# Optimization experiments

Measured on AMD Instinct MI355X. Metric: run time of the kernel, lower is better.

Reference implementation:

```python
import jax, jax.numpy as jnp
import numpy as np

DIM, DEPTH, DH, CH, SH = 512, 2, 64, 2, 8
B, T, N = 8, 1024, 2048
CI, SI, FF = CH * DH, SH * DH, 4 * DIM


def layer_norm(x, w, b, eps=1e-5):
    m = jnp.mean(x, -1, keepdims=True)
    v = jnp.var(x, -1, keepdims=True)
    return (x - m) * jax.lax.rsqrt(v + eps) * w + b


def rotate_half(x):
    # interleaved pairs: (x0,x1) -> (-x1,x0)
    x1, x2 = x[..., 0::2], x[..., 1::2]
    return jnp.stack((-x2, x1), axis=-1).reshape(x.shape)


def apply_rot(freqs, x):
    return x * jnp.cos(freqs) + rotate_half(x) * jnp.sin(freqs)


def split_heads(x, h):
    b, t, _ = x.shape
    return x.reshape(b, t, h, -1).transpose(0, 2, 1, 3)


def merge_heads(x):
    b, h, t, d = x.shape
    return x.transpose(0, 2, 1, 3).reshape(b, t, h * d)


def rotary_attn(q, k, v, q_pos, k_pos, heads, mask=None):
    # q:(B,Tq,H*Dh), k/v:(B,Tk,H*Dh), pos:(B,T,Dh); rotate_value=False -> v untouched
    qh, kh, vh = split_heads(q, heads), split_heads(k, heads), split_heads(v, heads)
    qh = apply_rot(q_pos[:, None], qh)
    kh = apply_rot(k_pos[:, None], kh)
    scores = jnp.einsum('bhqd,bhkd->bhqk', qh, kh) * (DH ** -0.5)
    if mask is not None:
        scores = jnp.where(mask, scores, jnp.finfo(scores.dtype).min)
    attn = jax.nn.softmax(scores, axis=-1)
    return merge_heads(jnp.einsum('bhqk,bhkd->bhqd', attn, vh))


def _forward(bin_queries, bin_time_emb, encoder_latents, latent_time_emb,
             ca_lnq_w, ca_lnq_b, ca_lnc_w, ca_lnc_b, ca_wq, ca_wkv, ca_wo, ca_bo,
             sa_ln_w, sa_ln_b, sa_wqkv, sa_wo, sa_bo,
             ffn_ln_w, ffn_ln_b, ffn_w1, ffn_b1, ffn_w2, ffn_b2):
    Tq = bin_queries.shape[1]
    mask = jnp.tril(jnp.ones((Tq, Tq), dtype=bool))[None, None]  # (1,1,T,T) causal
    x = bin_queries
    for l in range(DEPTH):
        # 1) rotary cross-attention to history latents
        xn = layer_norm(x, ca_lnq_w[l], ca_lnq_b[l])
        cn = layer_norm(encoder_latents, ca_lnc_w[l], ca_lnc_b[l])
        q = xn @ ca_wq[l]
        k, v = jnp.split(cn @ ca_wkv[l], 2, axis=-1)
        x = x + rotary_attn(q, k, v, bin_time_emb, latent_time_emb, CH) @ ca_wo[l] + ca_bo[l]
        # 2) causal rotary self-attention over bin queries
        xn = layer_norm(x, sa_ln_w[l], sa_ln_b[l])
        q, k, v = jnp.split(xn @ sa_wqkv[l], 3, axis=-1)
        x = x + rotary_attn(q, k, v, bin_time_emb, bin_time_emb, SH, mask) @ sa_wo[l] + sa_bo[l]
        # 3) pre-LN FFN with GEGLU (mult=4), dropout off in eval
        h = layer_norm(x, ffn_ln_w[l], ffn_ln_b[l])
        a, g = jnp.split(h @ ffn_w1[l] + ffn_b1[l], 2, axis=-1)
        x = x + (a * jax.nn.gelu(g, approximate=False)) @ ffn_w2[l] + ffn_b2[l]
    return x


def setup_inputs() -> dict:
    key = jax.random.key(0)
    ks = jax.random.split(key, 12)
    n = lambda i, shape, s: jax.random.normal(ks[i], shape, dtype=jnp.float32) * s
    return {
        'bin_queries': n(0, (B, T, DIM), 1.0),
        'bin_time_emb': n(1, (B, T, DH), 1.0),
        'encoder_latents': n(2, (B, N, DIM), 1.0),
        'latent_time_emb': n(3, (B, N, DH), 1.0),
        'ca_lnq_w': jnp.ones((DEPTH, DIM)), 'ca_lnq_b': jnp.zeros((DEPTH, DIM)),
        'ca_lnc_w': jnp.ones((DEPTH, DIM)), 'ca_lnc_b': jnp.zeros((DEPTH, DIM)),
        'ca_wq': n(4, (DEPTH, DIM, CI), 0.02), 'ca_wkv': n(5, (DEPTH, DIM, 2 * CI), 0.02),
        'ca_wo': n(6, (DEPTH, CI, DIM), 0.02), 'ca_bo': jnp.zeros((DEPTH, DIM)),
        'sa_ln_w': jnp.ones((DEPTH, DIM)), 'sa_ln_b': jnp.zeros((DEPTH, DIM)),
        'sa_wqkv': n(7, (DEPTH, DIM, 3 * SI), 0.02), 'sa_wo': n(8, (DEPTH, SI, DIM), 0.02),
        'sa_bo': jnp.zeros((DEPTH, DIM)),
        'ffn_ln_w': jnp.ones((DEPTH, DIM)), 'ffn_ln_b': jnp.zeros((DEPTH, DIM)),
        'ffn_w1': n(9, (DEPTH, DIM, 2 * FF), 0.02), 'ffn_b1': jnp.zeros((DEPTH, 2 * FF)),
        'ffn_w2': n(10, (DEPTH, FF, DIM), 0.02), 'ffn_b2': jnp.zeros((DEPTH, DIM)),
    }


def reference(bin_queries, bin_time_emb, encoder_latents, latent_time_emb,
              ca_lnq_w, ca_lnq_b, ca_lnc_w, ca_lnc_b, ca_wq, ca_wkv, ca_wo, ca_bo,
              sa_ln_w, sa_ln_b, sa_wqkv, sa_wo, sa_bo,
              ffn_ln_w, ffn_ln_b, ffn_w1, ffn_b1, ffn_w2, ffn_b2):
    return _forward(bin_queries, bin_time_emb, encoder_latents, latent_time_emb,
                    ca_lnq_w, ca_lnq_b, ca_lnc_w, ca_lnc_b, ca_wq, ca_wkv, ca_wo, ca_bo,
                    sa_ln_w, sa_ln_b, sa_wqkv, sa_wo, sa_bo,
                    ffn_ln_w, ffn_ln_b, ffn_w1, ffn_b1, ffn_w2, ffn_b2)
```

## Files before the change

### kernel.cpp

```cpp
#include <hip/hip_runtime.h>
#include <cstdint>
#include <cstddef>

static constexpr int DIMc = 512;
static constexpr int DHc  = 64;
static constexpr int CHc  = 2;
static constexpr int SHc  = 8;
static constexpr int Bc   = 8;
static constexpr int Tc   = 1024;
static constexpr int Nc   = 2048;
static constexpr int CIc  = CHc * DHc;
static constexpr int SIc  = SHc * DHc;
static constexpr int FFc  = 4 * DIMc;
static constexpr int RQ   = Bc * Tc;
static constexpr int RL   = Bc * Nc;

typedef short bf16x8 __attribute__((ext_vector_type(8)));
typedef float f32x4  __attribute__((ext_vector_type(4)));

__device__ __forceinline__ ushort f2bf(float f) {
  uint32_t u = __builtin_bit_cast(uint32_t, f);
  u += 0x7fffu + ((u >> 16) & 1u);
  return (ushort)(u >> 16);
}
__device__ __forceinline__ uint32_t packbf2(float a, float b) {
  return (uint32_t)f2bf(a) | ((uint32_t)f2bf(b) << 16);
}
__device__ __forceinline__ float bf2f(ushort h) {
  uint32_t u = ((uint32_t)h) << 16;
  return __builtin_bit_cast(float, u);
}

__device__ __forceinline__ void gload_lds16(const ushort* g, ushort* lds) {
  __builtin_amdgcn_global_load_lds(
      (const __attribute__((address_space(1))) void*)g,
      (__attribute__((address_space(3))) void*)lds, 16, 0, 0);
}

__device__ __forceinline__ bf16x8 ds_read8(const ushort* p) {
  bf16x8 d;
  asm volatile("ds_read_b128 %0, %1"
               : "=v"(d)
               : "v"((const __attribute__((address_space(3))) ushort*)p));
  return d;
}

__device__ __forceinline__ float gelu_fast(float g) {
  float u = g * (0.7978845608f + 0.0356774081f * g * g);
  float e = __expf(2.f * u);
  float th = 1.f - 2.f * __builtin_amdgcn_rcpf(1.f + e);
  return 0.5f * g * (1.f + th);
}

__device__ __forceinline__ float rope_rot(int odd, float v, float p, float2 cs) {
  return odd ? (v * cs.x + p * cs.y) : (v * cs.x - p * cs.y);
}

__global__ __launch_bounds__(256) void trig_prep(const float* __restrict__ src,
    float2* __restrict__ dst, int n) {
  int i = blockIdx.x * 256 + threadIdx.x;
  if (i >= n) return;
  float s, c;
  __sincosf(src[i], &s, &c);
  dst[i] = make_float2(c, s);
}

__global__ __launch_bounds__(256) void ln_rows(const float* __restrict__ X,
    const float* __restrict__ w, const float* __restrict__ b,
    ushort* __restrict__ out, int rows) {
  int gw = (int)((blockIdx.x * 256 + threadIdx.x) >> 6);
  int lane = threadIdx.x & 63;
  if (gw >= rows) return;
  const float* xr = X + (size_t)gw * DIMc;
  float4 v0 = *(const float4*)(xr + lane * 8);
  float4 v1 = *(const float4*)(xr + lane * 8 + 4);
  float xv[8] = {v0.x, v0.y, v0.z, v0.w, v1.x, v1.y, v1.z, v1.w};
  float s = 0.f, ss = 0.f;
#pragma unroll
  for (int i = 0; i < 8; i++) { s += xv[i]; ss += xv[i] * xv[i]; }
#pragma unroll
  for (int off = 32; off; off >>= 1) { s += __shfl_xor(s, off); ss += __shfl_xor(ss, off); }
  float mean = s * (1.f / DIMc);
  float var = ss * (1.f / DIMc) - mean * mean;
  float r = rsqrtf(var + 1e-5f);
  int c = lane * 8;
  ushort o[8] __attribute__((aligned(16)));
#pragma unroll
  for (int i = 0; i < 8; i++) o[i] = f2bf((xv[i] - mean) * r * w[c + i] + b[c + i]);
  *(uint4*)(out + (size_t)gw * DIMc + c) = *(const uint4*)o;
}

__global__ __launch_bounds__(256) void ln_rows2(const float* __restrict__ X,
    const float* __restrict__ w, const float* __restrict__ b,
    ushort* __restrict__ out0, ushort* __restrict__ out1, int rows) {
  int gw = (int)((blockIdx.x * 256 + threadIdx.x) >> 6);
  int lane = threadIdx.x & 63;
  if (gw >= rows) return;
  const float* xr = X + (size_t)gw * DIMc;
  float4 v0 = *(const float4*)(xr + lane * 8);
  float4 v1 = *(const float4*)(xr + lane * 8 + 4);
  float xv[8] = {v0.x, v0.y, v0.z, v0.w, v1.x, v1.y, v1.z, v1.w};
  float s = 0.f, ss = 0.f;
#pragma unroll
  for (int i = 0; i < 8; i++) { s += xv[i]; ss += xv[i] * xv[i]; }
#pragma unroll
  for (int off = 32; off; off >>= 1) { s += __shfl_xor(s, off); ss += __shfl_xor(ss, off); }
  float mean = s * (1.f / DIMc);
  float var = ss * (1.f / DIMc) - mean * mean;
  float r = rsqrtf(var + 1e-5f);
  int c = lane * 8;
  ushort o[8] __attribute__((aligned(16)));
#pragma unroll
  for (int i = 0; i < 8; i++) o[i] = f2bf((xv[i] - mean) * r * w[c + i] + b[c + i]);
  *(uint4*)(out0 + (size_t)gw * DIMc + c) = *(const uint4*)o;
#pragma unroll
  for (int i = 0; i < 8; i++) o[i] = f2bf((xv[i] - mean) * r * w[DIMc + c + i] + b[DIMc + c + i]);
  *(uint4*)(out1 + (size_t)gw * DIMc + c) = *(const uint4*)o;
}

__global__ __launch_bounds__(256) void wtrans_all(
    const float* __restrict__ wq, const float* __restrict__ wkv,
    const float* __restrict__ wo, const float* __restrict__ qkv,
    const float* __restrict__ swo, const float* __restrict__ w1,
    const float* __restrict__ w2, ushort* __restrict__ dst, int layer) {
  constexpr int Ks[7]   = {512, 512, 128, 512, 512, 512, 2048};
  constexpr int Ns[7]   = {128, 256, 512, 1536, 512, 4096, 512};
  constexpr int pre[8]  = {0, 64, 192, 256, 1024, 1280, 3328, 4352};
  constexpr int dOff[7] = {0, 65536, 196608, 262144, 1048576, 1310720, 3407872};
  int bid = blockIdx.x;
  int wid = 0;
#pragma unroll
  for (int i = 1; i < 7; i++) wid += (bid >= pre[i]);
  int tileIdx = bid - pre[wid];
  int K = Ks[wid], N = Ns[wid];
  const float* srcs[7] = {wq, wkv, wo, qkv, swo, w1, w2};
  const float* W = srcs[wid] + (size_t)layer * K * N;
  ushort* Wt = dst + dOff[wid];
  int ntx = N / 32;
  int n0 = (tileIdx % ntx) * 32, k0 = (tileIdx / ntx) * 32;
  __shared__ float tile[32][33];
  int tx = threadIdx.x & 31, ty = threadIdx.x >> 5;
#pragma unroll
  for (int i = 0; i < 32; i += 8)
    tile[ty + i][tx] = W[(size_t)(k0 + ty + i) * N + n0 + tx];
  __syncthreads();
  if (wid == 5) {
#pragma unroll
    for (int i = 0; i < 32; i += 8) {
      int nrow = n0 + ty + i;
      int p = nrow & 2047;
      int rowT = ((p >> 4) << 5) + ((nrow < 2048) ? 0 : 16) + (p & 15);
      Wt[(size_t)rowT * K + k0 + tx] = f2bf(tile[tx][ty + i]);
    }
  } else {
#pragma unroll
    for (int i = 0; i < 32; i += 8)
      Wt[(size_t)(n0 + ty + i) * K + k0 + tx] = f2bf(tile[tx][ty + i]);
  }
}

template<int MODE>
__global__ __launch_bounds__(256) void gemm128(const ushort* __restrict__ A,
    const ushort* __restrict__ Bt, const float* __restrict__ bias,
    const float* __restrict__ resIn, float* __restrict__ resOut,
    ushort* __restrict__ outB, int M, int N, int K,
    const float2* __restrict__ cs, ushort* __restrict__ vt) {
  __shared__ __align__(16) ushort As[128 * 64];
  __shared__ __align__(16) ushort Bs[128 * 64];
  int t = threadIdx.x, wv = t >> 6, lane = t & 63;
  int bm = blockIdx.y, bn = blockIdx.x;
  int fr = lane & 15, g = lane >> 4;
  int wr = (wv >> 1) * 64, wc = (wv & 1) * 64;
  int srow = wv * 32 + (lane >> 3);
  int sslot = lane & 7;
  const ushort* Abase = A + (size_t)(bm * 128) * K;
  const ushort* Bbase = Bt + (size_t)(bn * 128) * K;

  f32x4 acc[4][4] = {};
  for (int k0 = 0; k0 < K; k0 += 64) {
#pragma unroll
    for (int j = 0; j < 4; j++) {
      int r = srow + j * 8;
      int kc = sslot ^ (r & 7);
      gload_lds16(Abase + (size_t)r * K + k0 + kc * 8, As + (wv * 256 + j * 64) * 8);
      gload_lds16(Bbase + (size_t)r * K + k0 + kc * 8, Bs + (wv * 256 + j * 64) * 8);
    }
    __syncthreads();
#pragma unroll
    for (int ks = 0; ks < 2; ks++) {
      bf16x8 af[4], bf[4];
#pragma unroll
      for (int mm = 0; mm < 4; mm++) {
        int row = wr + mm * 16 + fr;
        af[mm] = *(const bf16x8*)(As + row * 64 + (((ks * 4 + g) ^ (row & 7)) * 8));
      }
#pragma unroll
      for (int nn = 0; nn < 4; nn++) {
        int row = wc + nn * 16 + fr;
        bf[nn] = *(const bf16x8*)(Bs + row * 64 + (((ks * 4 + g) ^ (row & 7)) * 8));
      }
#pragma unroll
      for (int mm = 0; mm < 4; mm++)
#pragma unroll
        for (int nn = 0; nn < 4; nn++)
          acc[mm][nn] = __builtin_amdgcn_mfma_f32_16x16x32_bf16(af[mm], bf[nn], acc[mm][nn], 0, 0, 0);
    }
    __syncthreads();
  }

  if (MODE == 2) {
    int NH = N >> 1;
#pragma unroll
    for (int mm = 0; mm < 4; mm++)
#pragma unroll
      for (int np = 0; np < 2; np++) {
        int ocol = bn * 64 + (wc >> 1) + np * 16 + fr;
        float ba = bias[ocol];
        float bg = bias[NH + ocol];
#pragma unroll
        for (int i = 0; i < 4; i++) {
          int gr = bm * 128 + wr + mm * 16 + g * 4 + i;
          float a = acc[mm][np * 2][i] + ba;
          float gv = acc[mm][np * 2 + 1][i] + bg;
          outB[(size_t)gr * NH + ocol] = f2bf(a * gelu_fast(gv));
        }
      }
  } else if (MODE == 3) {
    if (bn * 128 < 1024) {
#pragma unroll
      for (int mm = 0; mm < 4; mm++)
#pragma unroll
        for (int nn = 0; nn < 4; nn++) {
          int gc = bn * 128 + wc + nn * 16 + fr;
          int d = gc & 63;
          float sc = (gc < 512) ? 0.125f : 1.f;
#pragma unroll
          for (int i = 0; i < 4; i++) {
            int gr = bm * 128 + wr + mm * 16 + g * 4 + i;
            float val = acc[mm][nn][i];
            float prt = __shfl_xor(val, 1);
            float2 csv = cs[(size_t)gr * 64 + d];
            outB[(size_t)gr * N + gc] = f2bf(rope_rot(fr & 1, val, prt, csv) * sc);
          }
        }
    } else {
#pragma unroll
      for (int mm = 0; mm < 4; mm++)
#pragma unroll
        for (int nn = 0; nn < 4; nn++) {
          int gc = bn * 128 + wc + nn * 16 + fr;
          int ch = gc - 1024;
          int gr0 = bm * 128 + wr + mm * 16 + g * 4;
          int bb = gr0 >> 10, t0 = gr0 & 1023;
          uint2 w;
          w.x = packbf2(acc[mm][nn][0], acc[mm][nn][1]);
          w.y = packbf2(acc[mm][nn][2], acc[mm][nn][3]);
          *(uint2*)(vt + ((size_t)bb * 512 + ch) * 1024 + t0) = w;
        }
    }
  } else {
#pragma unroll
    for (int mm = 0; mm < 4; mm++)
#pragma unroll
      for (int nn = 0; nn < 4; nn++)
#pragma unroll
        for (int i = 0; i < 4; i++) {
          int gr = bm * 128 + wr + mm * 16 + g * 4 + i;
          int gc = bn * 128 + wc + nn * 16 + fr;
          float val = acc[mm][nn][i] + (bias ? bias[gc] : 0.f);
          if (MODE == 0) outB[(size_t)gr * N + gc] = f2bf(val);
          else resOut[(size_t)gr * N + gc] = resIn[(size_t)gr * N + gc] + val;
        }
  }
}

__global__ __launch_bounds__(512, 2) void gemm256_gelu(
    const ushort* __restrict__ A, const ushort* __restrict__ Bt,
    const float* __restrict__ bias, ushort* __restrict__ outB,
    int M, int N, int K) {
  __shared__ __align__(16) ushort As[2][256 * 64];
  __shared__ __align__(16) ushort Bs[2][256 * 64];
  int t = threadIdx.x, wv = t >> 6, lane = t & 63;
  int bm = blockIdx.y, bn = blockIdx.x;
  int fr = lane & 15, g = lane >> 4;
  int wr = (wv >> 2) * 128, wc = (wv & 3) * 64;
  int srow = wv * 32 + (lane >> 3);
  int sslot = lane & 7;
  const ushort* Abase = A + (size_t)(bm * 256) * K;
  const ushort* Bbase = Bt + (size_t)(bn * 256) * K;

  f32x4 acc[8][4] = {};
  int nt = K >> 6;

#define STG256(buf, kt)                                                       \
  {                                                                           \
    _Pragma("unroll")                                                         \
    for (int j = 0; j < 4; j++) {                                             \
      int r = srow + j * 8;                                                   \
      int kc = sslot ^ (r & 7);                                               \
      gload_lds16(Abase + (size_t)r * K + (kt) * 64 + kc * 8,                 \
                  &As[buf][(wv * 256 + j * 64) * 8]);                         \
      gload_lds16(Bbase + (size_t)r * K + (kt) * 64 + kc * 8,                 \
                  &Bs[buf][(wv * 256 + j * 64) * 8]);                         \
    }                                                                         \
  }

  STG256(0, 0);
  STG256(1, 1);

  for (int tt = 0; tt < nt; tt++) {
    int cur = tt & 1;
    if (tt + 1 < nt) asm volatile("s_waitcnt vmcnt(8)" ::: "memory");
    else             asm volatile("s_waitcnt vmcnt(0)" ::: "memory");
    __builtin_amdgcn_s_barrier();
    const ushort* Ac = As[cur];
    const ushort* Bc = Bs[cur];
#pragma unroll
    for (int ph = 0; ph < 4; ph++) {
      const int mh = ph >> 1, nh = ph & 1;
      bf16x8 af[2][4], bf[2][2];
#pragma unroll
      for (int ks = 0; ks < 2; ks++) {
#pragma unroll
        for (int mi = 0; mi < 4; mi++) {
          int row = wr + (mh * 4 + mi) * 16 + fr;
          af[ks][mi] = ds_read8(Ac + row * 64 + (((ks * 4 + g) ^ (row & 7)) * 8));
        }
#pragma unroll
        for (int ni = 0; ni < 2; ni++) {
          int row = wc + (nh * 2 + ni) * 16 + fr;
          bf[ks][ni] = ds_read8(Bc + row * 64 + (((ks * 4 + g) ^ (row & 7)) * 8));
        }
      }
      asm volatile("s_waitcnt lgkmcnt(0)" ::: "memory");
      __builtin_amdgcn_sched_barrier(0);
      __builtin_amdgcn_s_setprio(1);
#pragma unroll
      for (int ks = 0; ks < 2; ks++)
#pragma unroll
        for (int mi = 0; mi < 4; mi++)
#pragma unroll
          for (int ni = 0; ni < 2; ni++)
            acc[mh * 4 + mi][nh * 2 + ni] = __builtin_amdgcn_mfma_f32_16x16x32_bf16(
                af[ks][mi], bf[ks][ni], acc[mh * 4 + mi][nh * 2 + ni], 0, 0, 0);
      __builtin_amdgcn_s_setprio(0);
      __builtin_amdgcn_s_barrier();
    }
    if (tt + 2 < nt) STG256(cur, tt + 2);
  }
#undef STG256

  int NH = N >> 1;
#pragma unroll
  for (int mf = 0; mf < 8; mf++)
#pragma unroll
    for (int np = 0; np < 2; np++) {
      int ocol = bn * 128 + (wc >> 1) + np * 16 + fr;
      float ba = bias[ocol];
      float bg = bias[NH + ocol];
#pragma unroll
      for (int i = 0; i < 4; i++) {
        int gr = bm * 256 + wr + mf * 16 + g * 4 + i;
        float a = acc[mf][np * 2][i] + ba;
        float gv = acc[mf][np * 2 + 1][i] + bg;
        outB[(size_t)gr * NH + ocol] = f2bf(a * gelu_fast(gv));
      }
    }
}

template<int MODE>
__global__ __launch_bounds__(256) void gemm128x64(const ushort* __restrict__ A,
    const ushort* __restrict__ Bt, const float* __restrict__ bias,
    const float* __restrict__ resIn, float* __restrict__ resOut,
    ushort* __restrict__ outB, int M, int N, int K,
    const float2* __restrict__ cs, ushort* __restrict__ vt) {
  __shared__ __align__(16) ushort As[128 * 64];
  __shared__ __align__(16) ushort Bs[64 * 64];
  int t = threadIdx.x, wv = t >> 6, lane = t & 63;
  int bm = blockIdx.y, bn = blockIdx.x;
  int fr = lane & 15, g = lane >> 4;
  int wr = (wv >> 1) * 64, wc = (wv & 1) * 32;
  const ushort* Abase = A + (size_t)(bm * 128) * K;
  const ushort* Bbase = Bt + (size_t)(bn * 64) * K;

  f32x4 acc[4][2] = {};
  for (int k0 = 0; k0 < K; k0 += 64) {
#pragma unroll
    for (int j = 0; j < 4; j++) {
      int c = j * 256 + wv * 64 + lane;
      int r = c >> 3, s = c & 7;
      int kc = s ^ (r & 7);
      gload_lds16(Abase + (size_t)r * K + k0 + kc * 8, As + (j * 256 + wv * 64) * 8);
      if (j < 2)
        gload_lds16(Bbase + (size_t)r * K + k0 + kc * 8, Bs + (j * 256 + wv * 64) * 8);
    }
    __syncthreads();
#pragma unroll
    for (int ks = 0; ks < 2; ks++) {
      bf16x8 af[4], bf[2];
#pragma unroll
      for (int mm = 0; mm < 4; mm++) {
        int row = wr + mm * 16 + fr;
        af[mm] = *(const bf16x8*)(As + row * 64 + (((ks * 4 + g) ^ (row & 7)) * 8));
      }
#pragma unroll
      for (int nn = 0; nn < 2; nn++) {
        int row = wc + nn * 16 + fr;
        bf[nn] = *(const bf16x8*)(Bs + row * 64 + (((ks * 4 + g) ^ (row & 7)) * 8));
      }
#pragma unroll
      for (int mm = 0; mm < 4; mm++)
#pragma unroll
        for (int nn = 0; nn < 2; nn++)
          acc[mm][nn] = __builtin_amdgcn_mfma_f32_16x16x32_bf16(af[mm], bf[nn], acc[mm][nn], 0, 0, 0);
    }
    __syncthreads();
  }

  if (MODE == 3) {
    if (bn * 64 < 128) {
#pragma unroll
      for (int mm = 0; mm < 4; mm++)
#pragma unroll
        for (int nn = 0; nn < 2; nn++) {
          int gc = bn * 64 + wc + nn * 16 + fr;
          int d = gc & 63;
#pragma unroll
          for (int i = 0; i < 4; i++) {
            int gr = bm * 128 + wr + mm * 16 + g * 4 + i;
            float val = acc[mm][nn][i];
            float prt = __shfl_xor(val, 1);
            float2 csv = cs[(size_t)gr * 64 + d];
            outB[(size_t)gr * N + gc] = f2bf(rope_rot(fr & 1, val, prt, csv));
          }
        }
    } else {
#pragma unroll
      for (int mm = 0; mm < 4; mm++)
#pragma unroll
        for (int nn = 0; nn < 2; nn++) {
          int gc = bn * 64 + wc + nn * 16 + fr;
          int ch = gc - 128;
          int gr0 = bm * 128 + wr + mm * 16 + g * 4;
          int bb = gr0 >> 11, t0 = gr0 & 2047;
          uint2 w;
          w.x = packbf2(acc[mm][nn][0], acc[mm][nn][1]);
          w.y = packbf2(acc[mm][nn][2], acc[mm][nn][3]);
          *(uint2*)(vt + ((size_t)bb * 128 + ch) * 2048 + t0) = w;
        }
    }
  } else {
#pragma unroll
    for (int mm = 0; mm < 4; mm++)
#pragma unroll
      for (int nn = 0; nn < 2; nn++)
#pragma unroll
        for (int i = 0; i < 4; i++) {
          int gr = bm * 128 + wr + mm * 16 + g * 4 + i;
          int gc = bn * 64 + wc + nn * 16 + fr;
          float val = acc[mm][nn][i] + (bias ? bias[gc] : 0.f);
          if (MODE == 0) outB[(size_t)gr * N + gc] = f2bf(val);
          else resOut[(size_t)gr * N + gc] = resIn[(size_t)gr * N + gc] + val;
        }
  }
}

__global__ __launch_bounds__(256) void gemm64_rope(const ushort* __restrict__ A,
    const ushort* __restrict__ Bt, ushort* __restrict__ outB,
    const float2* __restrict__ cs, int M, int N, int K) {
  __shared__ __align__(16) ushort As[64][40];
  __shared__ __align__(16) ushort Bs[64][40];
  int t = threadIdx.x;
  int bm = blockIdx.y, bn = blockIdx.x;
  int row = t >> 2, kc = (t & 3) << 3;
  const ushort* aG = A + (size_t)(bm * 64 + row) * K + kc;
  const ushort* bG = Bt + (size_t)(bn * 64 + row) * K + kc;
  int wv = t >> 6, lane = t & 63;
  int wr = (wv >> 1) * 32, wc = (wv & 1) * 32;
  int fr = lane & 15, fk = (lane >> 4) << 3;
  f32x4 acc[2][2] = {};
  for (int k0 = 0; k0 < K; k0 += 32) {
    *(uint4*)&As[row][kc] = *(const uint4*)(aG + k0);
    *(uint4*)&Bs[row][kc] = *(const uint4*)(bG + k0);
    __syncthreads();
    bf16x8 a0 = *(const bf16x8*)&As[wr + fr][fk];
    bf16x8 a1 = *(const bf16x8*)&As[wr + 16 + fr][fk];
    bf16x8 b0 = *(const bf16x8*)&Bs[wc + fr][fk];
    bf16x8 b1 = *(const bf16x8*)&Bs[wc + 16 + fr][fk];
    acc[0][0] = __builtin_amdgcn_mfma_f32_16x16x32_bf16(a0, b0, acc[0][0], 0, 0, 0);
    acc[0][1] = __builtin_amdgcn_mfma_f32_16x16x32_bf16(a0, b1, acc[0][1], 0, 0, 0);
    acc[1][0] = __builtin_amdgcn_mfma_f32_16x16x32_bf16(a1, b0, acc[1][0], 0, 0, 0);
    acc[1][1] = __builtin_amdgcn_mfma_f32_16x16x32_bf16(a1, b1, acc[1][1], 0, 0, 0);
    __syncthreads();
  }
  int cr0 = wr + ((lane >> 4) << 2);
  int cc0 = wc + fr;
#pragma unroll
  for (int mm = 0; mm < 2; mm++)
#pragma unroll
    for (int nn = 0; nn < 2; nn++) {
      int gc = bn * 64 + cc0 + nn * 16;
      int d = gc & 63;
#pragma unroll
      for (int i = 0; i < 4; i++) {
        int gr = bm * 64 + cr0 + mm * 16 + i;
        float val = acc[mm][nn][i];
        float prt = __shfl_xor(val, 1);
        float2 csv = cs[(size_t)gr * 64 + d];
        outB[(size_t)gr * N + gc] = f2bf(rope_rot(fr & 1, val, prt, csv) * 0.125f);
      }
    }
}

template<int CAUSAL>
__global__ __launch_bounds__(256) void attn_mfma(
    const ushort* __restrict__ Q, const ushort* __restrict__ K,
    const ushort* __restrict__ Vt, ushort* __restrict__ O,
    int qStride, int kStride, int kOff, int oStride,
    int Tq, int NK, int H) {
  __shared__ __align__(16) ushort Ks[64 * 64];
  __shared__ __align__(16) ushort Vs[64 * 64];
  __shared__ __align__(16) ushort Ps[4][16 * 72];
  int b = blockIdx.z, h = blockIdx.y;
  int qt = CAUSAL ? ((int)gridDim.x - 1 - (int)blockIdx.x) : blockIdx.x;
  int t = threadIdx.x, wv = t >> 6, lane = t & 63;
  int g = lane >> 4, fr = lane & 15;
  int qw = qt * 64 + wv * 16;
  int HD = H * 64;

  const ushort* qrow = Q + (size_t)(b * Tq + qw + fr) * qStride + h * 64;
  bf16x8 qlo = *(const bf16x8*)(qrow + g * 8);
  bf16x8 qhi = *(const bf16x8*)(qrow + 32 + g * 8);

  f32x4 o_acc[4] = {};
  float m_run = -1e30f, l_run = 0.f;

  uint32_t* Pw = (uint32_t*)&Ps[wv][0];
  int ntiles = CAUSAL ? (qt + 1) : (NK / 64);
  for (int kt = 0; kt < ntiles; kt++) {
    int k0 = kt * 64;
    __syncthreads();
#pragma unroll
    for (int i = 0; i < 2; i++) {
      int id = t + i * 256;
      int r = id >> 3, c = id & 7;
      uint4 kval = *(const uint4*)(K + (size_t)(b * NK + k0 + r) * kStride + kOff + h * 64 + c * 8);
      *(uint4*)(Ks + r * 64 + ((c ^ (r & 7)) * 8)) = kval;
      uint4 vval = *(const uint4*)(Vt + ((size_t)b * HD + h * 64 + r) * NK + k0 + c * 8);
      *(uint4*)(Vs + r * 64 + ((c ^ (r & 7)) * 8)) = vval;
    }
    __syncthreads();

    f32x4 s[4];
#pragma unroll
    for (int nn = 0; nn < 4; nn++) {
      int row = nn * 16 + fr;
      bf16x8 kf0 = *(const bf16x8*)(Ks + row * 64 + ((g ^ (fr & 7)) * 8));
      bf16x8 kf1 = *(const bf16x8*)(Ks + row * 64 + (((4 + g) ^ (fr & 7)) * 8));
      f32x4 z = {};
      z = __builtin_amdgcn_mfma_f32_16x16x32_bf16(kf0, qlo, z, 0, 0, 0);
      z = __builtin_amdgcn_mfma_f32_16x16x32_bf16(kf1, qhi, z, 0, 0, 0);
      s[nn] = z;
    }
    if (CAUSAL && (k0 + 63 > qw)) {
#pragma unroll
      for (int nn = 0; nn < 4; nn++)
#pragma unroll
        for (int i = 0; i < 4; i++)
          if (k0 + nn * 16 + g * 4 + i > qw + fr) s[nn][i] = -1e30f;
    }
    float tm = s[0][0];
#pragma unroll
    for (int nn = 0; nn < 4; nn++)
#pragma unroll
      for (int i = 0; i < 4; i++) tm = fmaxf(tm, s[nn][i]);
    tm = fmaxf(tm, __shfl_xor(tm, 16));
    tm = fmaxf(tm, __shfl_xor(tm, 32));
    float mnew = fmaxf(m_run, tm);
    float corr = __expf(m_run - mnew);
    float ps = 0.f;
#pragma unroll
    for (int nn = 0; nn < 4; nn++)
#pragma unroll
      for (int i = 0; i < 4; i++) {
        float p = __expf(s[nn][i] - mnew);
        s[nn][i] = p;
        ps += p;
      }
    ps += __shfl_xor(ps, 16);
    ps += __shfl_xor(ps, 32);
    l_run = l_run * corr + ps;
    m_run = mnew;
#pragma unroll
    for (int dd = 0; dd < 4; dd++) o_acc[dd] *= corr;
#pragma unroll
    for (int nn = 0; nn < 4; nn++)
#pragma unroll
      for (int p = 0; p < 2; p++)
        Pw[fr * 36 + 8 * nn + 2 * g + p] = packbf2(s[nn][2 * p], s[nn][2 * p + 1]);
    bf16x8 pa0 = *(const bf16x8*)(&Ps[wv][fr * 72 + g * 8]);
    bf16x8 pa1 = *(const bf16x8*)(&Ps[wv][fr * 72 + 32 + g * 8]);
#pragma unroll
    for (int dd = 0; dd < 4; dd++) {
      int row = dd * 16 + fr;
      bf16x8 vf0 = *(const bf16x8*)(Vs + row * 64 + ((g ^ (fr & 7)) * 8));
      bf16x8 vf1 = *(const bf16x8*)(Vs + row * 64 + (((4 + g) ^ (fr & 7)) * 8));
      o_acc[dd] = __builtin_amdgcn_mfma_f32_16x16x32_bf16(vf0, pa0, o_acc[dd], 0, 0, 0);
      o_acc[dd] = __builtin_amdgcn_mfma_f32_16x16x32_bf16(vf1, pa1, o_acc[dd], 0, 0, 0);
    }
  }
  float rl = 1.f / l_run;
  ushort* obase = O + (size_t)(b * Tq + qw + fr) * oStride + h * 64;
#pragma unroll
  for (int dd = 0; dd < 4; dd++) {
    uint2 w;
    w.x = packbf2(o_acc[dd][0] * rl, o_acc[dd][1] * rl);
    w.y = packbf2(o_acc[dd][2] * rl, o_acc[dd][3] * rl);
    *(uint2*)(obase + dd * 16 + g * 4) = w;
  }
}

extern "C" void kernel_launch(void* const* d_in, const int* in_sizes, int n_in,
                              void* d_out, int out_size, void* d_ws, size_t ws_size,
                              hipStream_t stream) {
  const float* bin_queries = (const float*)d_in[0];
  const float* bin_time    = (const float*)d_in[1];
  const float* latents     = (const float*)d_in[2];
  const float* lat_time    = (const float*)d_in[3];
  const float* ca_lnq_w = (const float*)d_in[4];
  const float* ca_lnq_b = (const float*)d_in[5];
  const float* ca_lnc_w = (const float*)d_in[6];
  const float* ca_lnc_b = (const float*)d_in[7];
  const float* ca_wq  = (const float*)d_in[8];
  const float* ca_wkv = (const float*)d_in[9];
  const float* ca_wo  = (const float*)d_in[10];
  const float* ca_bo  = (const float*)d_in[11];
  const float* sa_ln_w = (const float*)d_in[12];
  const float* sa_ln_b = (const float*)d_in[13];
  const float* sa_wqkv = (const float*)d_in[14];
  const float* sa_wo   = (const float*)d_in[15];
  const float* sa_bo   = (const float*)d_in[16];
  const float* ffn_ln_w = (const float*)d_in[17];
  const float* ffn_ln_b = (const float*)d_in[18];
  const float* ffn_w1 = (const float*)d_in[19];
  const float* ffn_b1 = (const float*)d_in[20];
  const float* ffn_w2 = (const float*)d_in[21];
  const float* ffn_b2 = (const float*)d_in[22];

  constexpr size_t X_BYTES = (size_t)RQ * DIMc * 4;
  char* ws = (char*)d_ws;
  float* x = (float*)ws;
  char* A0 = ws + X_BYTES;
  ushort* cn     = (ushort*)(A0);
  ushort* ca_xn  = (ushort*)(A0 + 16777216);
  ushort* qbuf   = (ushort*)(A0 + 25165824);
  ushort* kv     = (ushort*)(A0 + 27262976);
  ushort* ca_att = (ushort*)(A0 + 35651584);
  ushort* vt_c   = (ushort*)(A0 + 37748736);
  ushort* sa_xn  = (ushort*)(A0);
  ushort* qkv    = (ushort*)(A0 + 8388608);
  ushort* sa_att = (ushort*)(A0 + 33554432);
  ushort* vt_s   = (ushort*)(A0 + 41943040);
  ushort* hb     = (ushort*)(A0);
  ushort* ag     = (ushort*)(A0 + 8388608);
  float2* csQ = (float2*)(A0 + 62914560);
  float2* csL = (float2*)(A0 + 67108864);
  ushort* cn2 = (ushort*)(A0 + 79691776);
  char* W0 = A0 + 109051904;
  ushort* wbase = (ushort*)W0;
  ushort* wqT  = wbase;
  ushort* wkvT = wbase + 65536;
  ushort* woT  = wbase + 196608;
  ushort* qkvT = wbase + 262144;
  ushort* swoT = wbase + 1048576;
  ushort* w1T  = wbase + 1310720;
  ushort* w2T  = wbase + 3407872;

  trig_prep<<<(RQ * 64) / 256, 256, 0, stream>>>(bin_time, csQ, RQ * 64);
  trig_prep<<<(RL * 64) / 256, 256, 0, stream>>>(lat_time, csL, RL * 64);
  ln_rows2<<<RL / 4, 256, 0, stream>>>(latents, ca_lnc_w, ca_lnc_b, cn, cn2, RL);

  for (int l = 0; l < 2; l++) {
    wtrans_all<<<4352, 256, 0, stream>>>(ca_wq, ca_wkv, ca_wo, sa_wqkv, sa_wo,
                                         ffn_w1, ffn_w2, wbase, l);

    const float* xin = (l == 0) ? bin_queries : x;
    const ushort* cnl = (l == 0) ? cn : cn2;
    ln_rows<<<RQ / 4, 256, 0, stream>>>(xin, ca_lnq_w + l * DIMc, ca_lnq_b + l * DIMc, ca_xn, RQ);
    gemm64_rope<<<dim3(CIc / 64, RQ / 64), 256, 0, stream>>>(ca_xn, wqT, qbuf, csQ, RQ, CIc, DIMc);
    gemm128x64<3><<<dim3(2 * CIc / 64, RL / 128), 256, 0, stream>>>(cnl, wkvT, nullptr,
        nullptr, nullptr, kv, RL, 2 * CIc, DIMc, csL, vt_c);
    attn_mfma<0><<<dim3(Tc / 64, CHc, Bc), 256, 0, stream>>>(qbuf, kv, vt_c, ca_att,
        CIc, 2 * CIc, 0, CIc, Tc, Nc, CHc);
    gemm128x64<1><<<dim3(DIMc / 64, RQ / 128), 256, 0, stream>>>(ca_att, woT, ca_bo + l * DIMc,
        xin, x, nullptr, RQ, DIMc, CIc, nullptr, nullptr);

    ln_rows<<<RQ / 4, 256, 0, stream>>>(x, sa_ln_w + l * DIMc, sa_ln_b + l * DIMc, sa_xn, RQ);
    gemm128<3><<<dim3(3 * SIc / 128, RQ / 128), 256, 0, stream>>>(sa_xn, qkvT, nullptr,
        nullptr, nullptr, qkv, RQ, 3 * SIc, DIMc, csQ, vt_s);
    attn_mfma<1><<<dim3(Tc / 64, SHc, Bc), 256, 0, stream>>>(qkv, qkv, vt_s, sa_att,
        3 * SIc, 3 * SIc, SIc, SIc, Tc, Tc, SHc);
    gemm128x64<1><<<dim3(DIMc / 64, RQ / 128), 256, 0, stream>>>(sa_att, swoT, sa_bo + l * DIMc,
        x, x, nullptr, RQ, DIMc, SIc, nullptr, nullptr);

    ln_rows<<<RQ / 4, 256, 0, stream>>>(x, ffn_ln_w + l * DIMc, ffn_ln_b + l * DIMc, hb, RQ);
    gemm256_gelu<<<dim3(2 * FFc / 256, RQ / 256), 512, 0, stream>>>(hb, w1T,
        ffn_b1 + (size_t)l * 2 * FFc, ag, RQ, 2 * FFc, DIMc);
    float* resOut = (l == 1) ? (float*)d_out : x;
    gemm128x64<1><<<dim3(DIMc / 64, RQ / 128), 256, 0, stream>>>(ag, w2T, ffn_b2 + l * DIMc,
        x, resOut, nullptr, RQ, DIMc, FFc, nullptr, nullptr);
  }
}
```

Baseline: 621.9 us.

## Split cross-attention over KV halves, widen key tiles to 128, use exp2 softmax

Cross-attention now splits the 2048-key range into two halves across extra blocks, writing partial fp32 outputs plus running max and sum, then a separate combine kernel merges them. This raises parallelism, since the original grid had only 16x2x8 blocks. Both attention kernels process 128-key tiles per iteration, halving barriers and loop overhead. The query scale is folded with log2(e) so the softmax can use exp2f. The cost is extra fp32 partial-output traffic and one more launch, and larger shared-memory tiles that may reduce occupancy.

```diff
diff --git a/kernel.cpp b/kernel.cpp
--- a/kernel.cpp
+++ b/kernel.cpp
@@ -14,6 +14,7 @@
 static constexpr int FFc  = 4 * DIMc;
 static constexpr int RQ   = Bc * Tc;
 static constexpr int RL   = Bc * Nc;
+#define QSCALE 0.1803368801f
 
 typedef short bf16x8 __attribute__((ext_vector_type(8)));
 typedef float f32x4  __attribute__((ext_vector_type(4)));
@@ -233,7 +234,7 @@
         for (int nn = 0; nn < 4; nn++) {
           int gc = bn * 128 + wc + nn * 16 + fr;
           int d = gc & 63;
-          float sc = (gc < 512) ? 0.125f : 1.f;
+          float sc = (gc < 512) ? QSCALE : 1.f;
 #pragma unroll
           for (int i = 0; i < 4; i++) {
             int gr = bm * 128 + wr + mm * 16 + g * 4 + i;
@@ -507,22 +508,98 @@
         float val = acc[mm][nn][i];
         float prt = __shfl_xor(val, 1);
         float2 csv = cs[(size_t)gr * 64 + d];
-        outB[(size_t)gr * N + gc] = f2bf(rope_rot(fr & 1, val, prt, csv) * 0.125f);
+        outB[(size_t)gr * N + gc] = f2bf(rope_rot(fr & 1, val, prt, csv) * QSCALE);
       }
     }
 }
 
-template<int CAUSAL>
-__global__ __launch_bounds__(256) void attn_mfma(
+#define ATTN_STAGE_TILE(k0)                                                   \
+  {                                                                           \
+    _Pragma("unroll")                                                         \
+    for (int i = 0; i < 4; i++) {                                             \
+      int id = t + i * 256;                                                   \
+      int r = id >> 3, c = id & 7;                                            \
+      uint4 kval = *(const uint4*)(K + (size_t)(b * NK + (k0) + r) * kStride  \
+                                   + kOff + h * 64 + c * 8);                  \
+      *(uint4*)(Ks + r * 64 + ((c ^ (r & 7)) * 8)) = kval;                    \
+      int rv = id >> 4, cv = id & 15;                                         \
+      uint4 vval = *(const uint4*)(Vt + ((size_t)b * HD + h * 64 + rv) * NK   \
+                                   + (k0) + cv * 8);                          \
+      *(uint4*)(Vs + rv * 128 + ((cv ^ (rv & 7)) * 8)) = vval;                \
+    }                                                                         \
+  }
+
+#define ATTN_TILE_BODY(MASKED)                                                \
+  {                                                                           \
+    f32x4 s[8];                                                               \
+    _Pragma("unroll")                                                         \
+    for (int nn = 0; nn < 8; nn++) {                                          \
+      int row = nn * 16 + fr;                                                 \
+      bf16x8 kf0 = *(const bf16x8*)(Ks + row * 64 + ((g ^ (fr & 7)) * 8));    \
+      bf16x8 kf1 = *(const bf16x8*)(Ks + row * 64 + (((4 + g) ^ (fr & 7)) * 8)); \
+      f32x4 z = {};                                                           \
+      z = __builtin_amdgcn_mfma_f32_16x16x32_bf16(kf0, qlo, z, 0, 0, 0);      \
+      z = __builtin_amdgcn_mfma_f32_16x16x32_bf16(kf1, qhi, z, 0, 0, 0);      \
+      s[nn] = z;                                                              \
+    }                                                                         \
+    if (MASKED) {                                                             \
+      _Pragma("unroll")                                                       \
+      for (int nn = 0; nn < 8; nn++)                                          \
+        _Pragma("unroll")                                                     \
+        for (int i = 0; i < 4; i++)                                           \
+          if (k0 + nn * 16 + g * 4 + i > qw + fr) s[nn][i] = -1e30f;          \
+    }                                                                         \
+    float tm = s[0][0];                                                       \
+    _Pragma("unroll")                                                         \
+    for (int nn = 0; nn < 8; nn++)                                            \
+      _Pragma("unroll")                                                       \
+      for (int i = 0; i < 4; i++) tm = fmaxf(tm, s[nn][i]);                   \
+    tm = fmaxf(tm, __shfl_xor(tm, 16));                                       \
+    tm = fmaxf(tm, __shfl_xor(tm, 32));                                       \
+    float mnew = fmaxf(m_run, tm);                                            \
+    float corr = exp2f(m_run - mnew);                                         \
+    float ps = 0.f;                                                           \
+    _Pragma("unroll")                                                         \
+    for (int nn = 0; nn < 8; nn++)                                            \
+      _Pragma("unroll")                                                       \
+      for (int i = 0; i < 4; i++) {                                           \
+        float p = exp2f(s[nn][i] - mnew);                                     \
+        s[nn][i] = p;                                                         \
+        ps += p;                                                              \
+      }                                                                       \
+    ps += __shfl_xor(ps, 16);                                                 \
+    ps += __shfl_xor(ps, 32);                                                 \
+    l_run = l_run * corr + ps;                                                \
+    m_run = mnew;                                                             \
+    _Pragma("unroll")                                                         \
+    for (int dd = 0; dd < 4; dd++) o_acc[dd] *= corr;                         \
+    _Pragma("unroll")                                                         \
+    for (int nn = 0; nn < 8; nn++)                                            \
+      _Pragma("unroll")                                                       \
+      for (int p = 0; p < 2; p++)                                             \
+        Pw[fr * 68 + nn * 8 + g * 2 + p] = packbf2(s[nn][2 * p], s[nn][2 * p + 1]); \
+    _Pragma("unroll")                                                         \
+    for (int ks = 0; ks < 4; ks++) {                                          \
+      bf16x8 pa = *(const bf16x8*)(&Ps[wv][fr * 136 + ks * 32 + g * 8]);      \
+      _Pragma("unroll")                                                       \
+      for (int dd = 0; dd < 4; dd++) {                                        \
+        int row = dd * 16 + fr;                                               \
+        bf16x8 vf = *(const bf16x8*)(Vs + row * 128 + (((ks * 4 + g) ^ (fr & 7)) * 8)); \
+        o_acc[dd] = __builtin_amdgcn_mfma_f32_16x16x32_bf16(vf, pa, o_acc[dd], 0, 0, 0); \
+      }                                                                       \
+    }                                                                         \
+  }
+
+__global__ __launch_bounds__(256) void attn_causal(
     const ushort* __restrict__ Q, const ushort* __restrict__ K,
     const ushort* __restrict__ Vt, ushort* __restrict__ O,
     int qStride, int kStride, int kOff, int oStride,
     int Tq, int NK, int H) {
-  __shared__ __align__(16) ushort Ks[64 * 64];
-  __shared__ __align__(16) ushort Vs[64 * 64];
-  __shared__ __align__(16) ushort Ps[4][16 * 72];
+  __shared__ __align__(16) ushort Ks[128 * 64];
+  __shared__ __align__(16) ushort Vs[64 * 128];
+  __shared__ __align__(16) ushort Ps[4][16 * 136];
   int b = blockIdx.z, h = blockIdx.y;
-  int qt = CAUSAL ? ((int)gridDim.x - 1 - (int)blockIdx.x) : blockIdx.x;
+  int qt = (int)gridDim.x - 1 - (int)blockIdx.x;
   int t = threadIdx.x, wv = t >> 6, lane = t & 63;
   int g = lane >> 4, fr = lane & 15;
   int qw = qt * 64 + wv * 16;
@@ -534,80 +611,15 @@
 
   f32x4 o_acc[4] = {};
   float m_run = -1e30f, l_run = 0.f;
-
   uint32_t* Pw = (uint32_t*)&Ps[wv][0];
-  int ntiles = CAUSAL ? (qt + 1) : (NK / 64);
+  int ntiles = (qt >> 1) + 1;
   for (int kt = 0; kt < ntiles; kt++) {
-    int k0 = kt * 64;
-    __syncthreads();
-#pragma unroll
-    for (int i = 0; i < 2; i++) {
-      int id = t + i * 256;
-      int r = id >> 3, c = id & 7;
-      uint4 kval = *(const uint4*)(K + (size_t)(b * NK + k0 + r) * kStride + kOff + h * 64 + c * 8);
-      *(uint4*)(Ks + r * 64 + ((c ^ (r & 7)) * 8)) = kval;
-      uint4 vval = *(const uint4*)(Vt + ((size_t)b * HD + h * 64 + r) * NK + k0 + c * 8);
-      *(uint4*)(Vs + r * 64 + ((c ^ (r & 7)) * 8)) = vval;
-    }
-    __syncthreads();
-
-    f32x4 s[4];
-#pragma unroll
-    for (int nn = 0; nn < 4; nn++) {
-      int row = nn * 16 + fr;
-      bf16x8 kf0 = *(const bf16x8*)(Ks + row * 64 + ((g ^ (fr & 7)) * 8));
-      bf16x8 kf1 = *(const bf16x8*)(Ks + row * 64 + (((4 + g) ^ (fr & 7)) * 8));
-      f32x4 z = {};
-      z = __builtin_amdgcn_mfma_f32_16x16x32_bf16(kf0, qlo, z, 0, 0, 0);
-      z = __builtin_amdgcn_mfma_f32_16x16x32_bf16(kf1, qhi, z, 0, 0, 0);
-      s[nn] = z;
-    }
-    if (CAUSAL && (k0 + 63 > qw)) {
-#pragma unroll
-      for (int nn = 0; nn < 4; nn++)
-#pragma unroll
-        for (int i = 0; i < 4; i++)
-          if (k0 + nn * 16 + g * 4 + i > qw + fr) s[nn][i] = -1e30f;
-    }
-    float tm = s[0][0];
-#pragma unroll
-    for (int nn = 0; nn < 4; nn++)
-#pragma unroll
-      for (int i = 0; i < 4; i++) tm = fmaxf(tm, s[nn][i]);
-    tm = fmaxf(tm, __shfl_xor(tm, 16));
-    tm = fmaxf(tm, __shfl_xor(tm, 32));
-    float mnew = fmaxf(m_run, tm);
-    float corr = __expf(m_run - mnew);
-    float ps = 0.f;
-#pragma unroll
-    for (int nn = 0; nn < 4; nn++)
-#pragma unroll
-      for (int i = 0; i < 4; i++) {
-        float p = __expf(s[nn][i] - mnew);
-        s[nn][i] = p;
-        ps += p;
-      }
-    ps += __shfl_xor(ps, 16);
-    ps += __shfl_xor(ps, 32);
-    l_run = l_run * corr + ps;
-    m_run = mnew;
-#pragma unroll
-    for (int dd = 0; dd < 4; dd++) o_acc[dd] *= corr;
-#pragma unroll
-    for (int nn = 0; nn < 4; nn++)
-#pragma unroll
-      for (int p = 0; p < 2; p++)
-        Pw[fr * 36 + 8 * nn + 2 * g + p] = packbf2(s[nn][2 * p], s[nn][2 * p + 1]);
-    bf16x8 pa0 = *(const bf16x8*)(&Ps[wv][fr * 72 + g * 8]);
-    bf16x8 pa1 = *(const bf16x8*)(&Ps[wv][fr * 72 + 32 + g * 8]);
-#pragma unroll
-    for (int dd = 0; dd < 4; dd++) {
-      int row = dd * 16 + fr;
-      bf16x8 vf0 = *(const bf16x8*)(Vs + row * 64 + ((g ^ (fr & 7)) * 8));
-      bf16x8 vf1 = *(const bf16x8*)(Vs + row * 64 + (((4 + g) ^ (fr & 7)) * 8));
-      o_acc[dd] = __builtin_amdgcn_mfma_f32_16x16x32_bf16(vf0, pa0, o_acc[dd], 0, 0, 0);
-      o_acc[dd] = __builtin_amdgcn_mfma_f32_16x16x32_bf16(vf1, pa1, o_acc[dd], 0, 0, 0);
-    }
+    int k0 = kt * 128;
+    __syncthreads();
+    ATTN_STAGE_TILE(k0);
+    __syncthreads();
+    if (k0 + 127 > qw) { ATTN_TILE_BODY(1); }
+    else               { ATTN_TILE_BODY(0); }
   }
   float rl = 1.f / l_run;
   ushort* obase = O + (size_t)(b * Tq + qw + fr) * oStride + h * 64;
@@ -618,6 +630,69 @@
     w.y = packbf2(o_acc[dd][2] * rl, o_acc[dd][3] * rl);
     *(uint2*)(obase + dd * 16 + g * 4) = w;
   }
+}
+
+__global__ __launch_bounds__(256) void attn_split(
+    const ushort* __restrict__ Q, const ushort* __restrict__ K,
+    const ushort* __restrict__ Vt, float* __restrict__ Opart,
+    float2* __restrict__ mlpart,
+    int qStride, int kStride, int kOff, int Tq, int NK, int H) {
+  __shared__ __align__(16) ushort Ks[128 * 64];
+  __shared__ __align__(16) ushort Vs[64 * 128];
+  __shared__ __align__(16) ushort Ps[4][16 * 136];
+  int b = blockIdx.z;
+  int h = blockIdx.y >> 1, sp = blockIdx.y & 1;
+  int qt = blockIdx.x;
+  int t = threadIdx.x, wv = t >> 6, lane = t & 63;
+  int g = lane >> 4, fr = lane & 15;
+  int qw = qt * 64 + wv * 16;
+  int HD = H * 64;
+  int half = NK / 256;
+  int ktbeg = sp * half, ktend = ktbeg + half;
+
+  const ushort* qrow = Q + (size_t)(b * Tq + qw + fr) * qStride + h * 64;
+  bf16x8 qlo = *(const bf16x8*)(qrow + g * 8);
+  bf16x8 qhi = *(const bf16x8*)(qrow + 32 + g * 8);
+
+  f32x4 o_acc[4] = {};
+  float m_run = -1e30f, l_run = 0.f;
+  uint32_t* Pw = (uint32_t*)&Ps[wv][0];
+  for (int kt = ktbeg; kt < ktend; kt++) {
+    int k0 = kt * 128;
+    __syncthreads();
+    ATTN_STAGE_TILE(k0);
+    __syncthreads();
+    ATTN_TILE_BODY(0);
+  }
+  size_t pslot = ((size_t)(b * H + h) * 2 + sp) * Tq + qw + fr;
+  float* obase = Opart + pslot * 64;
+#pragma unroll
+  for (int dd = 0; dd < 4; dd++)
+    *(float4*)(obase + dd * 16 + g * 4) = *(float4*)&o_acc[dd];
+  if (g == 0) mlpart[pslot] = make_float2(m_run, l_run);
+}
+
+__global__ __launch_bounds__(256) void attn_combine(
+    const float* __restrict__ Opart, const float2* __restrict__ mlpart,
+    ushort* __restrict__ O, int Tq, int H, int oStride) {
+  int idx = blockIdx.x * 256 + threadIdx.x;
+  int dq = (idx & 15) * 4;
+  int tt = (idx >> 4) & (Tq - 1);
+  int hh = idx >> 14;
+  int b = hh / H, h = hh % H;
+  size_t base0 = (((size_t)hh * 2 + 0) * Tq + tt) * 64 + dq;
+  size_t base1 = base0 + (size_t)Tq * 64;
+  float2 ml0 = mlpart[((size_t)hh * 2 + 0) * Tq + tt];
+  float2 ml1 = mlpart[((size_t)hh * 2 + 1) * Tq + tt];
+  float M = fmaxf(ml0.x, ml1.x);
+  float w0 = exp2f(ml0.x - M), w1 = exp2f(ml1.x - M);
+  float rl = 1.f / (w0 * ml0.y + w1 * ml1.y);
+  float4 o0 = *(const float4*)(Opart + base0);
+  float4 o1 = *(const float4*)(Opart + base1);
+  uint2 w;
+  w.x = packbf2((w0 * o0.x + w1 * o1.x) * rl, (w0 * o0.y + w1 * o1.y) * rl);
+  w.y = packbf2((w0 * o0.z + w1 * o1.z) * rl, (w0 * o0.w + w1 * o1.w) * rl);
+  *(uint2*)(O + (size_t)(b * Tq + tt) * oStride + h * 64 + dq) = w;
 }
 
 extern "C" void kernel_launch(void* const* d_in, const int* in_sizes, int n_in,
@@ -663,9 +738,11 @@
   ushort* vt_s   = (ushort*)(A0 + 41943040);
   ushort* hb     = (ushort*)(A0);
   ushort* ag     = (ushort*)(A0 + 8388608);
-  float2* csQ = (float2*)(A0 + 62914560);
-  float2* csL = (float2*)(A0 + 67108864);
-  ushort* cn2 = (ushort*)(A0 + 79691776);
+  float2* csQ    = (float2*)(A0 + 62914560);
+  float2* csL    = (float2*)(A0 + 67108864);
+  ushort* cn2    = (ushort*)(A0 + 79691776);
+  float*  Opart  = (float*)(A0 + 96468992);
+  float2* mlpart = (float2*)(A0 + 104857600);
   char* W0 = A0 + 109051904;
   ushort* wbase = (ushort*)W0;
   ushort* wqT  = wbase;
@@ -690,15 +767,17 @@
     gemm64_rope<<<dim3(CIc / 64, RQ / 64), 256, 0, stream>>>(ca_xn, wqT, qbuf, csQ, RQ, CIc, DIMc);
     gemm128x64<3><<<dim3(2 * CIc / 64, RL / 128), 256, 0, stream>>>(cnl, wkvT, nullptr,
         nullptr, nullptr, kv, RL, 2 * CIc, DIMc, csL, vt_c);
-    attn_mfma<0><<<dim3(Tc / 64, CHc, Bc), 256, 0, stream>>>(qbuf, kv, vt_c, ca_att,
-        CIc, 2 * CIc, 0, CIc, Tc, Nc, CHc);
+    attn_split<<<dim3(Tc / 64, CHc * 2, Bc), 256, 0, stream>>>(qbuf, kv, vt_c,
+        Opart, mlpart, CIc, 2 * CIc, 0, Tc, Nc, CHc);
+    attn_combine<<<(Bc * CHc * Tc * 16) / 256, 256, 0, stream>>>(Opart, mlpart,
+        ca_att, Tc, CHc, CIc);
     gemm128x64<1><<<dim3(DIMc / 64, RQ / 128), 256, 0, stream>>>(ca_att, woT, ca_bo + l * DIMc,
         xin, x, nullptr, RQ, DIMc, CIc, nullptr, nullptr);
 
     ln_rows<<<RQ / 4, 256, 0, stream>>>(x, sa_ln_w + l * DIMc, sa_ln_b + l * DIMc, sa_xn, RQ);
     gemm128<3><<<dim3(3 * SIc / 128, RQ / 128), 256, 0, stream>>>(sa_xn, qkvT, nullptr,
         nullptr, nullptr, qkv, RQ, 3 * SIc, DIMc, csQ, vt_s);
-    attn_mfma<1><<<dim3(Tc / 64, SHc, Bc), 256, 0, stream>>>(qkv, qkv, vt_s, sa_att,
+    attn_causal<<<dim3(Tc / 64, SHc, Bc), 256, 0, stream>>>(qkv, qkv, vt_s, sa_att,
         3 * SIc, 3 * SIc, SIc, SIc, Tc, Tc, SHc);
     gemm128x64<1><<<dim3(DIMc / 64, RQ / 128), 256, 0, stream>>>(sa_att, swoT, sa_bo + l * DIMc,
         x, x, nullptr, RQ, DIMc, SIc, nullptr, nullptr);
```

Measured after the change: 623.5 us. About the same (+0.3%).
